# Performance work log

Hardware: AMD Instinct MI355X
Metric: run time of the kernel (lower is better)

Reference implementation:

```python
import jax, jax.numpy as jnp
import numpy as np
import math

B, C, T = 2, 1024, 2048
H, G = 16, 32            # num_heads, groupnorm groups (channels=1024 -> 32 groups)
CH = C // H              # 64 head channels
EPS = 1e-5


def setup_inputs() -> dict:
    key = jax.random.key(0)
    ks = jax.random.split(key, 5)
    x = jax.random.normal(ks[0], (B, C, T), dtype=jnp.float32)
    # causal mask, identical across batch (matches how tortoise uses it; also makes
    # the torch mask.repeat(n_heads,1,1) tiling-order quirk a no-op)
    mask = jnp.broadcast_to(jnp.tril(jnp.ones((T, T), dtype=bool)), (B, T, T))
    qk_bias = jax.random.normal(ks[1], (1, T, T), dtype=jnp.float32) * 0.01
    gn_scale = jnp.ones((C,), dtype=jnp.float32)
    gn_bias = jnp.zeros((C,), dtype=jnp.float32)
    qkv_w = jax.random.normal(ks[2], (3 * C, C), dtype=jnp.float32) / math.sqrt(C)
    qkv_b = jnp.zeros((3 * C,), dtype=jnp.float32)
    # proj_out is zero-initialized in the module; use small random weights so the
    # attention path actually contributes (post-training regime)
    proj_w = jax.random.normal(ks[3], (C, C), dtype=jnp.float32) * 0.02
    proj_b = jnp.zeros((C,), dtype=jnp.float32)
    return {"x": x, "mask": mask, "qk_bias": qk_bias, "gn_scale": gn_scale,
            "gn_bias": gn_bias, "qkv_w": qkv_w, "qkv_b": qkv_b,
            "proj_w": proj_w, "proj_b": proj_b}


def _group_norm(x, scale, bias):
    # x: [B, C, T], normalize over (C//G, T) within each of G groups, in fp32
    xg = x.reshape(B, G, C // G, T)
    mean = xg.mean(axis=(2, 3), keepdims=True)
    var = ((xg - mean) ** 2).mean(axis=(2, 3), keepdims=True)
    xn = ((xg - mean) * jax.lax.rsqrt(var + EPS)).reshape(B, C, T)
    return xn * scale[None, :, None] + bias[None, :, None]


def reference(x, mask, qk_bias, gn_scale, gn_bias, qkv_w, qkv_b, proj_w, proj_b):
    xn = _group_norm(x, gn_scale, gn_bias)                      # [B, C, T]
    qkv = jnp.einsum('oc,bct->bot', qkv_w, xn) + qkv_b[None, :, None]  # [B, 3C, T]
    # legacy layout: width splits as (H, 3*ch)
    qkv = qkv.reshape(B * H, 3 * CH, T)
    q, k, v = qkv[:, :CH], qkv[:, CH:2 * CH], qkv[:, 2 * CH:]   # [B*H, ch, T]
    scale = 1.0 / math.sqrt(math.sqrt(CH))
    w = jnp.einsum('bct,bcs->bts', q * scale, k * scale)        # [B*H, T, T]
    w = w + qk_bias
    mask_r = jnp.tile(mask, (H, 1, 1))                          # matches torch repeat
    w = jnp.where(mask_r, w, -jnp.inf)
    w = jax.nn.softmax(w.astype(jnp.float32), axis=-1).astype(q.dtype)
    a = jnp.einsum('bts,bcs->bct', w, v).reshape(B, C, T)       # [B, C, T]
    h = jnp.einsum('oc,bct->bot', proj_w, a) + proj_b[None, :, None]
    return xn + h                                               # x_proj is Identity on normed x
```

## Files before the change

kernel.cpp:

```cpp
#include <hip/hip_runtime.h>
#include <stdint.h>

#define Tdim 2048
#define Cdim 1024
#define C3   3072

typedef __attribute__((ext_vector_type(8))) short s16x8;
typedef __attribute__((ext_vector_type(4))) unsigned short u16x4;
typedef __attribute__((ext_vector_type(2))) float f32x2;
typedef __attribute__((ext_vector_type(4))) float f32x4;
typedef __attribute__((ext_vector_type(16))) float f32x16;
typedef __attribute__((ext_vector_type(4))) int i32x4;

__device__ __forceinline__ unsigned short f2bf(float f) {
  uint32_t u = __float_as_uint(f);
  return (unsigned short)((u + 0x7FFFu + ((u >> 16) & 1u)) >> 16);
}
__device__ __forceinline__ float bf2f(unsigned short s) {
  return __uint_as_float(((uint32_t)s) << 16);
}
__device__ __forceinline__ uint32_t cvtpk(float lo, float hi) {
  uint32_t r;
  asm("v_cvt_pk_bf16_f32 %0, %1, %2" : "=v"(r) : "v"(lo), "v"(hi));
  return r;
}
__device__ __forceinline__ float exp2v(float x) {
  float r;
  asm("v_exp_f32 %0, %1" : "=v"(r) : "v"(x));
  return r;
}
typedef __attribute__((address_space(3))) unsigned char lds_uc;
typedef __attribute__((address_space(1))) const unsigned char glb_uc;
__device__ __forceinline__ void gload16(const void* g, void* l) {
  __builtin_amdgcn_global_load_lds((glb_uc*)g, (lds_uc*)l, 16, 0, 0);
}

__global__ __launch_bounds__(256) void k_gn_partial(const float* __restrict__ x,
                                                    float* __restrict__ part) {
  int bid = blockIdx.x;
  int bg = bid >> 3, tc = bid & 7;
  const float* xp = x + ((size_t)(bg >> 5) * Cdim + (size_t)(bg & 31) * 32) * Tdim + tc * 256;
  int u = threadIdx.x;
  float s1 = 0.f, s2 = 0.f;
#pragma unroll
  for (int i = 0; i < 32; ++i) {
    int e = u + i * 256;
    float v = xp[(size_t)(e >> 8) * Tdim + (e & 255)];
    s1 += v; s2 += v * v;
  }
  for (int m = 1; m < 64; m <<= 1) { s1 += __shfl_xor(s1, m); s2 += __shfl_xor(s2, m); }
  __shared__ float r1[4], r2[4];
  int w = u >> 6;
  if ((u & 63) == 0) { r1[w] = s1; r2[w] = s2; }
  __syncthreads();
  if (u == 0) {
    part[bid * 2]     = r1[0] + r1[1] + r1[2] + r1[3];
    part[bid * 2 + 1] = r2[0] + r2[1] + r2[2] + r2[3];
  }
}

__global__ void k_gn_final(const float* __restrict__ part, float* __restrict__ stats) {
  int bg = threadIdx.x;
  float s1 = 0.f, s2 = 0.f;
  for (int j = 0; j < 8; ++j) { s1 += part[(bg * 8 + j) * 2]; s2 += part[(bg * 8 + j) * 2 + 1]; }
  const float inv = 1.f / 65536.f;
  float mean = s1 * inv;
  float var = s2 * inv - mean * mean;
  stats[bg * 2] = mean;
  stats[bg * 2 + 1] = rsqrtf(var + 1e-5f);
}

__global__ __launch_bounds__(256) void k_gn_norm(const float* __restrict__ x,
                                                 const float* __restrict__ scale,
                                                 const float* __restrict__ bias,
                                                 const float* __restrict__ stats,
                                                 unsigned short* __restrict__ xnT) {
  int ti = blockIdx.x;
  int g  = blockIdx.y;
  int b  = blockIdx.z;
  int u  = threadIdx.x;
  int bg = b * 32 + g;
  float mean = stats[bg * 2], rstd = stats[bg * 2 + 1];
  __shared__ float L[32][65];
  int c_loc = u >> 3, tc = (u & 7) * 8;
  int cg = g * 32 + c_loc;
  const float* xp = x + ((size_t)b * Cdim + cg) * Tdim + ti * 64 + tc;
  float sc = scale[cg] * rstd;
  float bi = bias[cg] - mean * sc;
#pragma unroll
  for (int i = 0; i < 8; ++i) L[c_loc][tc + i] = xp[i] * sc + bi;
  __syncthreads();
  int t_loc = u >> 2, cc = (u & 3) * 8;
  s16x8 ov;
#pragma unroll
  for (int i = 0; i < 8; ++i) ov[i] = (short)f2bf(L[cc + i][t_loc]);
  *(s16x8*)&xnT[((size_t)b * Tdim + ti * 64 + t_loc) * Cdim + g * 32 + cc] = ov;
}

__global__ __launch_bounds__(256) void k_convert(const float* __restrict__ in,
                                                 unsigned short* __restrict__ out, int n4) {
  int i = blockIdx.x * 256 + threadIdx.x;
  if (i >= n4) return;
  f32x4 v = *(const f32x4*)(in + (size_t)i * 4);
  u16x4 o;
  o[0] = f2bf(v[0]); o[1] = f2bf(v[1]); o[2] = f2bf(v[2]); o[3] = f2bf(v[3]);
  *(u16x4*)(out + (size_t)i * 4) = o;
}

__global__ __launch_bounds__(256) void k_bias_t(const float* __restrict__ in,
                                                unsigned short* __restrict__ outT) {
  const float LOG2E = 1.4426950408889634f;
  int bs0 = blockIdx.x * 64;
  int bt0 = blockIdx.y * 64;
  __shared__ unsigned short L[64][65];
  int tid = threadIdx.x;
  int tl = tid >> 2, c0 = (tid & 3) * 16;
  const float* ip = in + (size_t)(bt0 + tl) * Tdim + bs0 + c0;
#pragma unroll
  for (int i = 0; i < 16; ++i) L[tl][c0 + i] = f2bf(ip[i] * LOG2E);
  __syncthreads();
  unsigned short* op = outT + (size_t)(bs0 + tl) * Tdim + bt0 + c0;
#pragma unroll
  for (int i = 0; i < 16; i += 4) {
    u16x4 o;
    o[0] = L[c0 + i][tl]; o[1] = L[c0 + i + 1][tl];
    o[2] = L[c0 + i + 2][tl]; o[3] = L[c0 + i + 3][tl];
    *(u16x4*)(op + i) = o;
  }
}

__global__ __launch_bounds__(256) void k_qkv(const unsigned short* __restrict__ A,
                                             const unsigned short* __restrict__ Bw,
                                             const float* __restrict__ bias,
                                             unsigned short* __restrict__ outT) {
  const int M = 2048, N = 3072, K = 1024;
  int bx = blockIdx.x, by = blockIdx.y, bb = blockIdx.z;
  int tid = threadIdx.x;
  int lane = tid & 63, w = tid >> 6;
  int m0 = by * 128, n0 = bx * 128;
  const unsigned short* Ab = A + (size_t)bb * M * K;
  __shared__ __align__(16) short As[128 * 32];
  __shared__ __align__(16) short Bs[128 * 32];
  f32x4 acc[4][4] = {};
  int wm = (w >> 1) * 64, wn = (w & 1) * 64;
  int lr = lane & 15, lq = lane >> 4;
  int srow = w * 16 + (lane >> 2);
  int scol = (lane & 3) * 8;

  for (int k0 = 0; k0 < K; k0 += 32) {
    __syncthreads();
#pragma unroll
    for (int ch = 0; ch < 2; ++ch) {
      gload16(Ab + (size_t)(m0 + srow + ch * 64) * K + k0 + scol,
              (char*)As + w * 1024 + ch * 4096);
      gload16(Bw + (size_t)(n0 + srow + ch * 64) * K + k0 + scol,
              (char*)Bs + w * 1024 + ch * 4096);
    }
    __syncthreads();
    s16x8 af[4], bfr[4];
#pragma unroll
    for (int m = 0; m < 4; ++m) af[m] = *(const s16x8*)&As[(wm + m * 16 + lr) * 32 + lq * 8];
#pragma unroll
    for (int n = 0; n < 4; ++n) bfr[n] = *(const s16x8*)&Bs[(wn + n * 16 + lr) * 32 + lq * 8];
#pragma unroll
    for (int m = 0; m < 4; ++m)
#pragma unroll
      for (int n = 0; n < 4; ++n)
        acc[m][n] = __builtin_amdgcn_mfma_f32_16x16x32_bf16(af[m], bfr[n], acc[m][n], 0, 0, 0);
  }
#pragma unroll
  for (int n = 0; n < 4; ++n) {
    int col = n0 + wn + n * 16 + lr;
    float bv = bias[col];
#pragma unroll
    for (int m = 0; m < 4; ++m) {
      int rowb = m0 + wm + m * 16 + lq * 4;
#pragma unroll
      for (int j = 0; j < 4; ++j)
        outT[((size_t)bb * M + rowb + j) * N + col] = f2bf(acc[m][n][j] + bv);
    }
  }
}

__global__ __launch_bounds__(256) void k_proj(const unsigned short* __restrict__ A,
                                              const unsigned short* __restrict__ Bw,
                                              const float* __restrict__ bias,
                                              const unsigned short* __restrict__ xnT,
                                              float* __restrict__ out) {
  const int K = 1024;
  int n0 = blockIdx.x * 64, m0 = blockIdx.y * 128;
  int tid = threadIdx.x;
  int lane = tid & 63, w = tid >> 6;
  __shared__ __align__(16) short As[128 * 32];
  __shared__ __align__(16) short Bs[64 * 32];
  f32x4 acc[4][2] = {};
  int wm = (w & 1) * 64, wn = (w >> 1) * 32;
  int lr = lane & 15, lq = lane >> 4;
  int srow = w * 16 + (lane >> 2);
  int scol = (lane & 3) * 8;

  for (int k0 = 0; k0 < K; k0 += 32) {
    __syncthreads();
#pragma unroll
    for (int ch = 0; ch < 2; ++ch)
      gload16(A + (size_t)(m0 + srow + ch * 64) * K + k0 + scol,
              (char*)As + w * 1024 + ch * 4096);
    gload16(Bw + (size_t)(n0 + srow) * K + k0 + scol, (char*)Bs + w * 1024);
    __syncthreads();
    s16x8 af[4], bfr[2];
#pragma unroll
    for (int m = 0; m < 4; ++m) af[m] = *(const s16x8*)&As[(wm + m * 16 + lr) * 32 + lq * 8];
#pragma unroll
    for (int n = 0; n < 2; ++n) bfr[n] = *(const s16x8*)&Bs[(wn + n * 16 + lr) * 32 + lq * 8];
#pragma unroll
    for (int m = 0; m < 4; ++m)
#pragma unroll
      for (int n = 0; n < 2; ++n)
        acc[m][n] = __builtin_amdgcn_mfma_f32_16x16x32_bf16(af[m], bfr[n], acc[m][n], 0, 0, 0);
  }
#pragma unroll
  for (int n = 0; n < 2; ++n) {
    int col = n0 + wn + n * 16 + lr;
    float bv = bias[col];
#pragma unroll
    for (int m = 0; m < 4; ++m) {
      int rowb = m0 + wm + m * 16 + lq * 4;
      int bb = rowb >> 11, t = rowb & 2047;
      f32x4 v;
#pragma unroll
      for (int j = 0; j < 4; ++j)
        v[j] = acc[m][n][j] + bv + bf2f(xnT[(size_t)(rowb + j) * Cdim + col]);
      *(f32x4*)&out[((size_t)bb * 1024 + col) * Tdim + t] = v;
    }
  }
}

__global__ __launch_bounds__(256, 2) void k_attn(const unsigned short* __restrict__ qkvT,
                                                 const unsigned short* __restrict__ biasT,
                                                 unsigned short* __restrict__ part0,
                                                 unsigned short* __restrict__ part1,
                                                 unsigned short* __restrict__ part2,
                                                 float* __restrict__ ml) {
  int x = blockIdx.x;
  int ti, cc, nc;
  if (x < 15)      { ti = 15 - x / 3;        cc = x - (x / 3) * 3;  nc = 3; }
  else if (x < 27) { int y = x - 15; ti = 10 - (y >> 1); cc = y & 1; nc = 2; }
  else             { ti = 31 - x;            cc = 0;               nc = 1; }
  int nt_tot = 2 * ti + 2;
  int bse = nt_tot / nc, rem = nt_tot - bse * nc;
  int start = cc * bse + (cc < rem ? cc : rem);
  int cnt = bse + (cc < rem ? 1 : 0);

  int bh = blockIdx.y;
  int b = bh >> 4, h = bh & 15;
  int tid = threadIdx.x, lane = tid & 63, w = tid >> 6;
  int r = lane & 31, hi = lane >> 5;
  int q0 = ti * 128 + w * 32;
  int qg = q0 + r;
  const unsigned short* hb = qkvT + ((size_t)b * Tdim) * C3 + h * 192;
  const unsigned short* bT = biasT + qg;
  unsigned short* pout = (cc == 0) ? part0 : (cc == 1) ? part1 : part2;

  __shared__ __align__(16) char Ks[2][8192];
  __shared__ __align__(16) char Vt[2][8192];

  s16x8 qf[4];
#pragma unroll
  for (int kb = 0; kb < 4; ++kb) {
    s16x8 raw = *(const s16x8*)(hb + (size_t)qg * C3 + kb * 16 + hi * 8);
#pragma unroll
    for (int j = 0; j < 8; ++j)
      qf[kb][j] = (short)f2bf(bf2f((unsigned short)raw[j]) * 0.18033688011114373f);
  }

  int ksr[2], kcb[2], vsr[2], vc0[2];
#pragma unroll
  for (int p = 0; p < 2; ++p) {
    int u = tid + p * 256;
    ksr[p] = u >> 3; kcb[p] = u & 7;
    vsr[p] = u & 63; vc0[p] = (u >> 6) * 8;
  }
  s16x8 kc[2], vc[2];
  unsigned short bs[2][16];

  auto issue_kv = [&](int s0) {
#pragma unroll
    for (int p = 0; p < 2; ++p) {
      kc[p] = *(const s16x8*)(hb + (size_t)(s0 + ksr[p]) * C3 + 64 + kcb[p] * 8);
      vc[p] = *(const s16x8*)(hb + (size_t)(s0 + vsr[p]) * C3 + 128 + vc0[p]);
    }
  };
  auto issue_bias = [&](int s0) {
#pragma unroll
    for (int st = 0; st < 2; ++st)
#pragma unroll
      for (int e = 0; e < 16; ++e) {
        int s = s0 + st * 32 + (e & 3) + 8 * (e >> 2) + 4 * hi;
        bs[st][e] = bT[(size_t)s * Tdim];
      }
  };

  issue_kv(start * 64);
  issue_bias(start * 64);

  f32x16 oacc[2];
#pragma unroll
  for (int c2 = 0; c2 < 2; ++c2)
#pragma unroll
    for (int e = 0; e < 16; ++e) oacc[c2][e] = 0.f;
  float mrow = -1e30f, lrowv = 0.f;

  for (int it = 0; it < cnt; ++it) {
    int s0 = (start + it) * 64;
    int cur = it & 1;
    char* Kc = &Ks[cur][0];
    char* Vc = &Vt[cur][0];
#pragma unroll
    for (int p = 0; p < 2; ++p) {
      *(s16x8*)(Kc + ksr[p] * 128 + ((kcb[p] * 16) ^ ((ksr[p] & 7) << 4))) = kc[p];
#pragma unroll
      for (int i = 0; i < 8; ++i)
        *(short*)(Vc + (vc0[p] + i) * 128 + ((vsr[p] * 2) ^ (((vc0[p] + i) & 7) << 4))) = vc[p][i];
    }
    __syncthreads();
    if (it + 1 < cnt) issue_kv(s0 + 64);

    bool active = (s0 <= q0 + 31);
    if (active) {
      f32x16 sa[2];
#pragma unroll
      for (int st = 0; st < 2; ++st) {
#pragma unroll
        for (int e = 0; e < 16; ++e) sa[st][e] = bf2f(bs[st][e]);
        int row = st * 32 + r;
        int swz = (row & 7) << 4;
        __builtin_amdgcn_s_setprio(1);
#pragma unroll
        for (int kb = 0; kb < 4; ++kb) {
          s16x8 kf = *(const s16x8*)(Kc + row * 128 + ((kb * 32 + hi * 16) ^ swz));
          sa[st] = __builtin_amdgcn_mfma_f32_32x32x16_bf16(kf, qf[kb], sa[st], 0, 0, 0);
        }
        __builtin_amdgcn_s_setprio(0);
      }
      if (s0 + 63 > q0) {
#pragma unroll
        for (int st = 0; st < 2; ++st)
#pragma unroll
          for (int e = 0; e < 16; ++e) {
            int s = s0 + st * 32 + (e & 3) + 8 * (e >> 2) + 4 * hi;
            sa[st][e] = (s > qg) ? -1e30f : sa[st][e];
          }
      }
      if (it + 1 < cnt && s0 + 64 <= q0 + 31) issue_bias(s0 + 64);
      float t8[8];
#pragma unroll
      for (int e = 0; e < 8; ++e)
        t8[e] = fmaxf(fmaxf(sa[0][e], sa[0][e + 8]), fmaxf(sa[1][e], sa[1][e + 8]));
      float pm = fmaxf(fmaxf(fmaxf(t8[0], t8[1]), fmaxf(t8[2], t8[3])),
                       fmaxf(fmaxf(t8[4], t8[5]), fmaxf(t8[6], t8[7])));
      pm = fmaxf(pm, __shfl_xor(pm, 32));
      if (!__all(pm <= mrow + 11.5f)) {
        float mnew = fmaxf(mrow, pm);
        float al = exp2v(mrow - mnew);
        mrow = mnew;
        lrowv *= al;
#pragma unroll
        for (int c2 = 0; c2 < 2; ++c2)
#pragma unroll
          for (int e = 0; e < 16; ++e) oacc[c2][e] *= al;
      }
#pragma unroll
      for (int st = 0; st < 2; ++st)
#pragma unroll
        for (int e = 0; e < 16; ++e) sa[st][e] = exp2v(sa[st][e] - mrow);
      float s8[8];
#pragma unroll
      for (int e = 0; e < 8; ++e)
        s8[e] = (sa[0][e] + sa[0][e + 8]) + (sa[1][e] + sa[1][e + 8]);
      float rsum = ((s8[0] + s8[1]) + (s8[2] + s8[3])) + ((s8[4] + s8[5]) + (s8[6] + s8[7]));
      rsum += __shfl_xor(rsum, 32);
      lrowv += rsum;

      s16x8 pfr[4];
#pragma unroll
      for (int sblk = 0; sblk < 4; ++sblk) {
        const int st = sblk >> 1, sb = sblk & 1;
        uint32_t a0 = cvtpk(sa[st][sb * 8 + 0], sa[st][sb * 8 + 1]);
        uint32_t a1 = cvtpk(sa[st][sb * 8 + 2], sa[st][sb * 8 + 3]);
        uint32_t b0 = cvtpk(sa[st][sb * 8 + 4], sa[st][sb * 8 + 5]);
        uint32_t b1 = cvtpk(sa[st][sb * 8 + 6], sa[st][sb * 8 + 7]);
        uint32_t xa0 = (uint32_t)__shfl_xor((int)a0, 32);
        uint32_t xa1 = (uint32_t)__shfl_xor((int)a1, 32);
        uint32_t xb0 = (uint32_t)__shfl_xor((int)b0, 32);
        uint32_t xb1 = (uint32_t)__shfl_xor((int)b1, 32);
        union { i32x4 i; s16x8 s; } u;
        u.i[0] = (int)(hi ? xb0 : a0);
        u.i[1] = (int)(hi ? xb1 : a1);
        u.i[2] = (int)(hi ? b0 : xa0);
        u.i[3] = (int)(hi ? b1 : xa1);
        pfr[sblk] = u.s;
      }
      __builtin_amdgcn_s_setprio(1);
#pragma unroll
      for (int c2 = 0; c2 < 2; ++c2) {
        int row = c2 * 32 + r;
        int swz = (row & 7) << 4;
#pragma unroll
        for (int sblk = 0; sblk < 4; ++sblk) {
          s16x8 vf = *(const s16x8*)(Vc + row * 128 + ((sblk * 32 + hi * 16) ^ swz));
          oacc[c2] = __builtin_amdgcn_mfma_f32_32x32x16_bf16(vf, pfr[sblk], oacc[c2], 0, 0, 0);
        }
      }
      __builtin_amdgcn_s_setprio(0);
    }
  }

  unsigned short* ob = pout + ((size_t)b * Tdim + qg) * Cdim + h * 64;
#pragma unroll
  for (int c2 = 0; c2 < 2; ++c2)
#pragma unroll
    for (int rg = 0; rg < 4; ++rg) {
      u16x4 o;
#pragma unroll
      for (int j = 0; j < 4; ++j) o[j] = f2bf(oacc[c2][rg * 4 + j]);
      *(u16x4*)(ob + c2 * 32 + rg * 8 + 4 * hi) = o;
    }
  if (hi == 0)
    *(f32x2*)(ml + ((size_t)(cc * 32 + bh) * Tdim + qg) * 2) = f32x2{mrow, lrowv};
}

__global__ __launch_bounds__(256) void k_merge(unsigned short* __restrict__ part0,
                                               const unsigned short* __restrict__ part1,
                                               const unsigned short* __restrict__ part2,
                                               const float* __restrict__ ml) {
  int idx = blockIdx.x * 256 + threadIdx.x;
  int ch8 = idx & 7;
  int q = (idx >> 3) & 2047;
  int bh = idx >> 14;
  int b = bh >> 4, h = bh & 15;
  int ti = q >> 7;
  int nc = (ti >= 11) ? 3 : (ti >= 5) ? 2 : 1;
  size_t off = ((size_t)b * Tdim + q) * Cdim + h * 64 + ch8 * 8;
  s16x8 o0 = *(const s16x8*)(part0 + off);
  f32x2 ml0 = *(const f32x2*)(ml + ((size_t)bh * Tdim + q) * 2);
  if (nc == 1) {
    float inv = 1.0f / ml0[1];
    s16x8 o;
#pragma unroll
    for (int i = 0; i < 8; ++i) o[i] = (short)f2bf(bf2f((unsigned short)o0[i]) * inv);
    *(s16x8*)(part0 + off) = o;
    return;
  }
  f32x2 ml1 = *(const f32x2*)(ml + ((size_t)(32 + bh) * Tdim + q) * 2);
  s16x8 o1 = *(const s16x8*)(part1 + off);
  float m = fmaxf(ml0[0], ml1[0]);
  f32x2 ml2;
  s16x8 o2;
  if (nc == 3) {
    ml2 = *(const f32x2*)(ml + ((size_t)(64 + bh) * Tdim + q) * 2);
    o2 = *(const s16x8*)(part2 + off);
    m = fmaxf(m, ml2[0]);
  }
  float e0 = exp2f(ml0[0] - m), e1 = exp2f(ml1[0] - m);
  float den = ml0[1] * e0 + ml1[1] * e1;
  float e2 = 0.f;
  if (nc == 3) { e2 = exp2f(ml2[0] - m); den += ml2[1] * e2; }
  float inv = 1.0f / den;
  float w0 = e0 * inv, w1 = e1 * inv, w2 = e2 * inv;
  s16x8 o;
#pragma unroll
  for (int i = 0; i < 8; ++i) {
    float v = bf2f((unsigned short)o0[i]) * w0 + bf2f((unsigned short)o1[i]) * w1;
    if (nc == 3) v += bf2f((unsigned short)o2[i]) * w2;
    o[i] = (short)f2bf(v);
  }
  *(s16x8*)(part0 + off) = o;
}

extern "C" void kernel_launch(void* const* d_in, const int* in_sizes, int n_in,
                              void* d_out, int out_size, void* d_ws, size_t ws_size,
                              hipStream_t stream) {
  const float* x        = (const float*)d_in[0];
  const float* qk_bias  = (const float*)d_in[2];
  const float* gn_scale = (const float*)d_in[3];
  const float* gn_bias  = (const float*)d_in[4];
  const float* qkv_w    = (const float*)d_in[5];
  const float* qkv_b    = (const float*)d_in[6];
  const float* proj_w   = (const float*)d_in[7];
  const float* proj_b   = (const float*)d_in[8];
  float* out = (float*)d_out;

  char* ws = (char*)d_ws;
  unsigned short* xnT   = (unsigned short*)(ws);
  unsigned short* qkvT  = (unsigned short*)(ws + ( 8ull << 20));
  unsigned short* aT    = (unsigned short*)(ws + (32ull << 20));
  unsigned short* part1 = (unsigned short*)(ws + (40ull << 20));
  unsigned short* wqkv  = (unsigned short*)(ws + (40ull << 20));
  unsigned short* wproj = (unsigned short*)(ws + (48ull << 20));
  float*          ml    = (float*)(ws + (50ull << 20));
  float* part  = (float*)(ws + (52ull << 20));
  float* stats = (float*)(ws + (52ull << 20) + 8192);
  unsigned short* biasT = (unsigned short*)d_out;
  unsigned short* part2 = (unsigned short*)d_out + (4ull << 20);

  k_gn_partial<<<512, 256, 0, stream>>>(x, part);
  k_gn_final<<<1, 64, 0, stream>>>(part, stats);
  k_gn_norm<<<dim3(32, 32, 2), 256, 0, stream>>>(x, gn_scale, gn_bias, stats, xnT);

  k_convert<<<(3072 * 1024 / 4 + 255) / 256, 256, 0, stream>>>(qkv_w, wqkv, 3072 * 1024 / 4);
  k_convert<<<(1024 * 1024 / 4 + 255) / 256, 256, 0, stream>>>(proj_w, wproj, 1024 * 1024 / 4);
  k_bias_t<<<dim3(32, 32), 256, 0, stream>>>(qk_bias, biasT);

  k_qkv<<<dim3(24, 16, 2), 256, 0, stream>>>(xnT, wqkv, qkv_b, qkvT);
  k_attn<<<dim3(32, 32), 256, 0, stream>>>(qkvT, biasT, aT, part1, part2, ml);
  k_merge<<<2048, 256, 0, stream>>>(aT, part1, part2, ml);
  k_proj<<<dim3(16, 32), 256, 0, stream>>>(aT, wproj, proj_b, xnT, out);
}
```

Measured before the change: 150.4 us.

## Double-buffer GEMM LDS tiles and load attention K tiles directly to LDS

The QKV and output-projection GEMMs move to double-buffered LDS tiles. The next K-slice is fetched with direct global-to-LDS loads while MFMAs run on the current buffer, which drops one barrier per iteration. In the attention kernel, K tiles now go straight into the swizzled LDS buffer through gload16 instead of passing through registers, with the swizzle applied on the source address. This costs twice the LDS for the GEMMs and relies on the swizzled source mapping and the barrier placement being correct for the asynchronous loads.

```diff
diff --git a/kernel.cpp b/kernel.cpp
--- a/kernel.cpp
+++ b/kernel.cpp
@@ -139,34 +139,40 @@
   int lane = tid & 63, w = tid >> 6;
   int m0 = by * 128, n0 = bx * 128;
   const unsigned short* Ab = A + (size_t)bb * M * K;
-  __shared__ __align__(16) short As[128 * 32];
-  __shared__ __align__(16) short Bs[128 * 32];
+  __shared__ __align__(16) short As[2][128 * 32];
+  __shared__ __align__(16) short Bs[2][128 * 32];
   f32x4 acc[4][4] = {};
   int wm = (w >> 1) * 64, wn = (w & 1) * 64;
   int lr = lane & 15, lq = lane >> 4;
   int srow = w * 16 + (lane >> 2);
   int scol = (lane & 3) * 8;
 
-  for (int k0 = 0; k0 < K; k0 += 32) {
-    __syncthreads();
+  auto stage = [&](int k0, int buf) {
 #pragma unroll
     for (int ch = 0; ch < 2; ++ch) {
       gload16(Ab + (size_t)(m0 + srow + ch * 64) * K + k0 + scol,
-              (char*)As + w * 1024 + ch * 4096);
+              (char*)&As[buf][0] + w * 1024 + ch * 4096);
       gload16(Bw + (size_t)(n0 + srow + ch * 64) * K + k0 + scol,
-              (char*)Bs + w * 1024 + ch * 4096);
-    }
-    __syncthreads();
+              (char*)&Bs[buf][0] + w * 1024 + ch * 4096);
+    }
+  };
+
+  stage(0, 0);
+  __syncthreads();
+  for (int kk = 0; kk < K / 32; ++kk) {
+    int cur = kk & 1;
+    if (kk + 1 < K / 32) stage((kk + 1) * 32, cur ^ 1);
     s16x8 af[4], bfr[4];
 #pragma unroll
-    for (int m = 0; m < 4; ++m) af[m] = *(const s16x8*)&As[(wm + m * 16 + lr) * 32 + lq * 8];
-#pragma unroll
-    for (int n = 0; n < 4; ++n) bfr[n] = *(const s16x8*)&Bs[(wn + n * 16 + lr) * 32 + lq * 8];
+    for (int m = 0; m < 4; ++m) af[m] = *(const s16x8*)&As[cur][(wm + m * 16 + lr) * 32 + lq * 8];
+#pragma unroll
+    for (int n = 0; n < 4; ++n) bfr[n] = *(const s16x8*)&Bs[cur][(wn + n * 16 + lr) * 32 + lq * 8];
 #pragma unroll
     for (int m = 0; m < 4; ++m)
 #pragma unroll
       for (int n = 0; n < 4; ++n)
         acc[m][n] = __builtin_amdgcn_mfma_f32_16x16x32_bf16(af[m], bfr[n], acc[m][n], 0, 0, 0);
+    __syncthreads();
   }
 #pragma unroll
   for (int n = 0; n < 4; ++n) {
@@ -191,32 +197,38 @@
   int n0 = blockIdx.x * 64, m0 = blockIdx.y * 128;
   int tid = threadIdx.x;
   int lane = tid & 63, w = tid >> 6;
-  __shared__ __align__(16) short As[128 * 32];
-  __shared__ __align__(16) short Bs[64 * 32];
+  __shared__ __align__(16) short As[2][128 * 32];
+  __shared__ __align__(16) short Bs[2][64 * 32];
   f32x4 acc[4][2] = {};
   int wm = (w & 1) * 64, wn = (w >> 1) * 32;
   int lr = lane & 15, lq = lane >> 4;
   int srow = w * 16 + (lane >> 2);
   int scol = (lane & 3) * 8;
 
-  for (int k0 = 0; k0 < K; k0 += 32) {
-    __syncthreads();
+  auto stage = [&](int k0, int buf) {
 #pragma unroll
     for (int ch = 0; ch < 2; ++ch)
       gload16(A + (size_t)(m0 + srow + ch * 64) * K + k0 + scol,
-              (char*)As + w * 1024 + ch * 4096);
-    gload16(Bw + (size_t)(n0 + srow) * K + k0 + scol, (char*)Bs + w * 1024);
-    __syncthreads();
+              (char*)&As[buf][0] + w * 1024 + ch * 4096);
+    gload16(Bw + (size_t)(n0 + srow) * K + k0 + scol, (char*)&Bs[buf][0] + w * 1024);
+  };
+
+  stage(0, 0);
+  __syncthreads();
+  for (int kk = 0; kk < K / 32; ++kk) {
+    int cur = kk & 1;
+    if (kk + 1 < K / 32) stage((kk + 1) * 32, cur ^ 1);
     s16x8 af[4], bfr[2];
 #pragma unroll
-    for (int m = 0; m < 4; ++m) af[m] = *(const s16x8*)&As[(wm + m * 16 + lr) * 32 + lq * 8];
-#pragma unroll
-    for (int n = 0; n < 2; ++n) bfr[n] = *(const s16x8*)&Bs[(wn + n * 16 + lr) * 32 + lq * 8];
+    for (int m = 0; m < 4; ++m) af[m] = *(const s16x8*)&As[cur][(wm + m * 16 + lr) * 32 + lq * 8];
+#pragma unroll
+    for (int n = 0; n < 2; ++n) bfr[n] = *(const s16x8*)&Bs[cur][(wn + n * 16 + lr) * 32 + lq * 8];
 #pragma unroll
     for (int m = 0; m < 4; ++m)
 #pragma unroll
       for (int n = 0; n < 2; ++n)
         acc[m][n] = __builtin_amdgcn_mfma_f32_16x16x32_bf16(af[m], bfr[n], acc[m][n], 0, 0, 0);
+    __syncthreads();
   }
 #pragma unroll
   for (int n = 0; n < 2; ++n) {
@@ -273,22 +285,32 @@
       qf[kb][j] = (short)f2bf(bf2f((unsigned short)raw[j]) * 0.18033688011114373f);
   }
 
-  int ksr[2], kcb[2], vsr[2], vc0[2];
+  int ks_s[2], ks_src[2];
+#pragma unroll
+  for (int p = 0; p < 2; ++p) {
+    ks_s[p] = p * 32 + (tid >> 3);
+    int colp = (tid & 7) * 16;
+    ks_src[p] = (colp ^ ((ks_s[p] & 7) << 4)) >> 1;
+  }
+  int vsr[2], vc0[2];
 #pragma unroll
   for (int p = 0; p < 2; ++p) {
     int u = tid + p * 256;
-    ksr[p] = u >> 3; kcb[p] = u & 7;
     vsr[p] = u & 63; vc0[p] = (u >> 6) * 8;
   }
-  s16x8 kc[2], vc[2];
+  s16x8 vc[2];
   unsigned short bs[2][16];
 
-  auto issue_kv = [&](int s0) {
-#pragma unroll
-    for (int p = 0; p < 2; ++p) {
-      kc[p] = *(const s16x8*)(hb + (size_t)(s0 + ksr[p]) * C3 + 64 + kcb[p] * 8);
+  auto issue_k = [&](int s0, char* Kbuf) {
+#pragma unroll
+    for (int p = 0; p < 2; ++p)
+      gload16(hb + (size_t)(s0 + ks_s[p]) * C3 + 64 + ks_src[p],
+              Kbuf + w * 1024 + p * 4096);
+  };
+  auto issue_v = [&](int s0) {
+#pragma unroll
+    for (int p = 0; p < 2; ++p)
       vc[p] = *(const s16x8*)(hb + (size_t)(s0 + vsr[p]) * C3 + 128 + vc0[p]);
-    }
   };
   auto issue_bias = [&](int s0) {
 #pragma unroll
@@ -300,7 +322,8 @@
       }
   };
 
-  issue_kv(start * 64);
+  issue_k(start * 64, &Ks[0][0]);
+  issue_v(start * 64);
   issue_bias(start * 64);
 
   f32x16 oacc[2];
@@ -317,13 +340,15 @@
     char* Vc = &Vt[cur][0];
 #pragma unroll
     for (int p = 0; p < 2; ++p) {
-      *(s16x8*)(Kc + ksr[p] * 128 + ((kcb[p] * 16) ^ ((ksr[p] & 7) << 4))) = kc[p];
 #pragma unroll
       for (int i = 0; i < 8; ++i)
         *(short*)(Vc + (vc0[p] + i) * 128 + ((vsr[p] * 2) ^ (((vc0[p] + i) & 7) << 4))) = vc[p][i];
     }
     __syncthreads();
-    if (it + 1 < cnt) issue_kv(s0 + 64);
+    if (it + 1 < cnt) {
+      issue_k(s0 + 64, &Ks[cur ^ 1][0]);
+      issue_v(s0 + 64);
+    }
 
     bool active = (s0 <= q0 + 31);
     if (active) {
```

New measurement: 166.7 us. +10.8%, slower.

## Remap GEMM and attention block indices for XCD-local L2 reuse; merge weight converts

Applied to the files above, without the earlier changes.

Block indices in the QKV GEMM, projection GEMM and attention kernels are remapped so that blocks landing on the same XCD (round-robin by linear block id mod 8) share A/B tiles or heads. The aim is more L2 reuse per XCD and less traffic to HBM or the Infinity Fabric. The two weight-conversion launches are also fused into one kernel, saving one launch. The remapping changes scheduling order and could unbalance the causal attention work across XCDs.

```diff
diff --git a/kernel.cpp b/kernel.cpp
--- a/kernel.cpp
+++ b/kernel.cpp
@@ -97,10 +97,15 @@
   *(s16x8*)&xnT[((size_t)b * Tdim + ti * 64 + t_loc) * Cdim + g * 32 + cc] = ov;
 }
 
-__global__ __launch_bounds__(256) void k_convert(const float* __restrict__ in,
-                                                 unsigned short* __restrict__ out, int n4) {
+__global__ __launch_bounds__(256) void k_convert_w(const float* __restrict__ in0,
+                                                   const float* __restrict__ in1,
+                                                   unsigned short* __restrict__ out0,
+                                                   unsigned short* __restrict__ out1) {
+  const int n0 = 3072 * 1024 / 4;
   int i = blockIdx.x * 256 + threadIdx.x;
-  if (i >= n4) return;
+  const float* in = in0;
+  unsigned short* out = out0;
+  if (i >= n0) { i -= n0; in = in1; out = out1; }
   f32x4 v = *(const f32x4*)(in + (size_t)i * 4);
   u16x4 o;
   o[0] = f2bf(v[0]); o[1] = f2bf(v[1]); o[2] = f2bf(v[2]); o[3] = f2bf(v[3]);
@@ -134,7 +139,12 @@
                                              const float* __restrict__ bias,
                                              unsigned short* __restrict__ outT) {
   const int M = 2048, N = 3072, K = 1024;
-  int bx = blockIdx.x, by = blockIdx.y, bb = blockIdx.z;
+  int lin = blockIdx.x + 24 * (blockIdx.y + 16 * blockIdx.z);
+  int k8 = lin & 7, j = lin >> 3;
+  int bb = k8 >> 2;
+  int q = k8 & 3;
+  int by = (q >> 1) * 8 + j / 12;
+  int bx = (q & 1) * 12 + j % 12;
   int tid = threadIdx.x;
   int lane = tid & 63, w = tid >> 6;
   int m0 = by * 128, n0 = bx * 128;
@@ -176,8 +186,8 @@
     for (int m = 0; m < 4; ++m) {
       int rowb = m0 + wm + m * 16 + lq * 4;
 #pragma unroll
-      for (int j = 0; j < 4; ++j)
-        outT[((size_t)bb * M + rowb + j) * N + col] = f2bf(acc[m][n][j] + bv);
+      for (int j2 = 0; j2 < 4; ++j2)
+        outT[((size_t)bb * M + rowb + j2) * N + col] = f2bf(acc[m][n][j2] + bv);
     }
   }
 }
@@ -188,7 +198,11 @@
                                               const unsigned short* __restrict__ xnT,
                                               float* __restrict__ out) {
   const int K = 1024;
-  int n0 = blockIdx.x * 64, m0 = blockIdx.y * 128;
+  int lin = blockIdx.x + 16 * blockIdx.y;
+  int k8 = lin & 7, j = lin >> 3;
+  int mt = (k8 >> 1) * 8 + (j >> 3);
+  int nt = (k8 & 1) * 8 + (j & 7);
+  int n0 = nt * 64, m0 = mt * 128;
   int tid = threadIdx.x;
   int lane = tid & 63, w = tid >> 6;
   __shared__ __align__(16) short As[128 * 32];
@@ -228,8 +242,8 @@
       int bb = rowb >> 11, t = rowb & 2047;
       f32x4 v;
 #pragma unroll
-      for (int j = 0; j < 4; ++j)
-        v[j] = acc[m][n][j] + bv + bf2f(xnT[(size_t)(rowb + j) * Cdim + col]);
+      for (int j2 = 0; j2 < 4; ++j2)
+        v[j2] = acc[m][n][j2] + bv + bf2f(xnT[(size_t)(rowb + j2) * Cdim + col]);
       *(f32x4*)&out[((size_t)bb * 1024 + col) * Tdim + t] = v;
     }
   }
@@ -241,7 +255,10 @@
                                                  unsigned short* __restrict__ part1,
                                                  unsigned short* __restrict__ part2,
                                                  float* __restrict__ ml) {
-  int x = blockIdx.x;
+  int lin = blockIdx.x + 32 * blockIdx.y;
+  int k8 = lin & 7, j8 = lin >> 3;
+  int bh = k8 * 4 + (j8 >> 5);
+  int x  = j8 & 31;
   int ti, cc, nc;
   if (x < 15)      { ti = 15 - x / 3;        cc = x - (x / 3) * 3;  nc = 3; }
   else if (x < 27) { int y = x - 15; ti = 10 - (y >> 1); cc = y & 1; nc = 2; }
@@ -251,7 +268,6 @@
   int start = cc * bse + (cc < rem ? cc : rem);
   int cnt = bse + (cc < rem ? 1 : 0);
 
-  int bh = blockIdx.y;
   int b = bh >> 4, h = bh & 15;
   int tid = threadIdx.x, lane = tid & 63, w = tid >> 6;
   int r = lane & 31, hi = lane >> 5;
@@ -507,8 +523,7 @@
   k_gn_final<<<1, 64, 0, stream>>>(part, stats);
   k_gn_norm<<<dim3(32, 32, 2), 256, 0, stream>>>(x, gn_scale, gn_bias, stats, xnT);
 
-  k_convert<<<(3072 * 1024 / 4 + 255) / 256, 256, 0, stream>>>(qkv_w, wqkv, 3072 * 1024 / 4);
-  k_convert<<<(1024 * 1024 / 4 + 255) / 256, 256, 0, stream>>>(proj_w, wproj, 1024 * 1024 / 4);
+  k_convert_w<<<4096, 256, 0, stream>>>(qkv_w, proj_w, wqkv, wproj);
   k_bias_t<<<dim3(32, 32), 256, 0, stream>>>(qk_bias, biasT);
 
   k_qkv<<<dim3(24, 16, 2), 256, 0, stream>>>(xnT, wqkv, qkv_b, qkvT);
```

After: 142.3 us. -5.4%, faster.
